# Performance work log

Hardware: AMD Instinct MI355X
Metric: run time of the kernel (lower is better)

Reference implementation:

```python
import jax, jax.numpy as jnp
import numpy as np

B, S, PLM, G = 8, 2048, 768, 256
N_WM, E_WM = 50000, 800000
N_F, E_F = B * S, 131072
K = 4


def _gnn(h, src, dst, Ws, bs, n_nodes):
    # simple GCN-style message passing: aggregate neighbor features via
    # gather (h[src]) + scatter-add (segment_sum), then linear + relu.
    for W, b in zip(Ws, bs):
        m = jax.ops.segment_sum(h[src], dst, num_segments=n_nodes)  # [n, g]
        h = jax.nn.relu((h + m) @ W + b)
    return h


def setup_inputs() -> dict:
    key = jax.random.key(0)
    ks = jax.random.split(key, 16)
    std = 0.02
    inp = {
        "text_embeddings": jax.random.normal(ks[0], (B, S, PLM), jnp.float32),
        "wm_x": jax.random.normal(ks[1], (N_WM, G), jnp.float32),
        "wm_edge_index": jax.random.randint(ks[2], (2, E_WM), 0, N_WM),
        "token2nodepos": jax.random.randint(ks[3], (B * S, K), 0, N_WM),
        "fstm_node_ids": jax.random.randint(ks[4], (N_F,), 0, N_F),
        "fstm_edge_index": jax.random.randint(ks[5], (2, E_F), 0, N_F),
        # extra_emb: nn.Embedding(2, G, padding_idx=0) -> row 0 is zeros
        "extra_emb": jax.random.normal(ks[6], (2, G), jnp.float32).at[0].set(0.0) * std,
        "wm_W1": jax.random.normal(ks[7], (G, G), jnp.float32) * std,
        "wm_b1": jnp.zeros((G,), jnp.float32),
        "wm_W2": jax.random.normal(ks[8], (G, G), jnp.float32) * std,
        "wm_b2": jnp.zeros((G,), jnp.float32),
        "fstm_W1": jax.random.normal(ks[9], (G, G), jnp.float32) * std,
        "fstm_b1": jnp.zeros((G,), jnp.float32),
        "fstm_W2": jax.random.normal(ks[10], (G, G), jnp.float32) * std,
        "fstm_b2": jnp.zeros((G,), jnp.float32),
        "fc1_W": jax.random.normal(ks[11], (G + PLM, G), jnp.float32) * std,
        "fc1_b": jnp.zeros((G,), jnp.float32),
        "fc3_W": jax.random.normal(ks[12], (PLM + 2 * G, PLM), jnp.float32) * std,
        "fc3_b": jnp.zeros((PLM,), jnp.float32),
    }
    return inp


def reference(text_embeddings, wm_x, wm_edge_index, token2nodepos, fstm_node_ids,
              fstm_edge_index, extra_emb, wm_W1, wm_b1, wm_W2, wm_b2,
              fstm_W1, fstm_b1, fstm_W2, fstm_b2, fc1_W, fc1_b, fc3_W, fc3_b):
    # ====== WM ======
    graph_embeddings = _gnn(wm_x, wm_edge_index[0], wm_edge_index[1],
                            (wm_W1, wm_W2), (wm_b1, wm_b2), N_WM)  # [N_WM, G]
    table = jnp.concatenate([extra_emb, graph_embeddings], axis=0)  # [N_WM+2, G]
    # per-token gather-sum over K concept slots (original python loop, vectorized)
    tmp = jnp.sum(table[token2nodepos + 2], axis=1)  # [B*S, G]
    text_flat = text_embeddings.reshape(B * S, PLM)
    graph_text_embed = jnp.concatenate([tmp, text_flat], axis=-1) @ fc1_W + fc1_b  # [B*S, G]
    # ====== FSTM ======
    x = graph_text_embed[fstm_node_ids]  # [B*S, G]
    temporal = _gnn(x, fstm_edge_index[0], fstm_edge_index[1],
                    (fstm_W1, fstm_W2), (fstm_b1, fstm_b2), N_F)
    temporal = temporal.reshape(B, S, G)
    # ====== Final ======
    final_vec = jnp.concatenate(
        [text_embeddings, tmp.reshape(B, S, G), temporal], axis=-1)
    logits = final_vec @ fc3_W + fc3_b  # [B, S, PLM]
    return logits
```

## Files before the change

kernel.cpp:

```cpp
#include <hip/hip_runtime.h>

#define Bsz 8
#define Ssz 2048
#define PLM 768
#define Gd  256
#define N_WM 50000
#define E_WM 800000
#define N_F  16384
#define E_F  131072
#define Kc   4

typedef unsigned short ushort_t;
typedef unsigned int uint_t;
typedef short short8 __attribute__((ext_vector_type(8)));
typedef float f32x4 __attribute__((ext_vector_type(4)));

__device__ __forceinline__ ushort_t f2bf(float f) {
    union { float f; unsigned int u; } v; v.f = f;
    unsigned int r = (v.u + 0x7fffu + ((v.u >> 16) & 1u)) >> 16;
    return (ushort_t)r;
}
__device__ __forceinline__ float bf2f(ushort_t b) {
    union { unsigned int u; float f; } v; v.u = ((unsigned int)b) << 16;
    return v.f;
}
__device__ __forceinline__ float4 bf4f(ushort4 u) {
    return make_float4(bf2f(u.x), bf2f(u.y), bf2f(u.z), bf2f(u.w));
}

__device__ __forceinline__ void gl2lds16(const ushort_t* g, ushort_t* l) {
    __builtin_amdgcn_global_load_lds(
        (const __attribute__((address_space(1))) unsigned int*)g,
        (__attribute__((address_space(3))) unsigned int*)l, 16, 0, 0);
}

#define NSL 8
#define SLW 32

__device__ __forceinline__ void cvt4(const float* __restrict__ in,
                                     ushort_t* __restrict__ out, int i, int n4) {
    if (i < n4) {
        float4 v = ((const float4*)in)[i];
        ushort4 u;
        u.x = f2bf(v.x); u.y = f2bf(v.y); u.z = f2bf(v.z); u.w = f2bf(v.w);
        ((ushort4*)out)[i] = u;
    }
}

__device__ __forceinline__ void cvt4_sm(const float* __restrict__ in,
                                        ushort_t* __restrict__ out, int i, int n4,
                                        int nrows) {
    if (i < n4) {
        float4 v = ((const float4*)in)[i];
        int flat = i * 4;
        int node = flat >> 8, c = flat & 255;
        int s = c >> 5, cc = c & 31;
        ushort4 u;
        u.x = f2bf(v.x); u.y = f2bf(v.y); u.z = f2bf(v.z); u.w = f2bf(v.w);
        *(ushort4*)&out[((size_t)s * nrows + node) * SLW + cc] = u;
    }
}

__device__ __forceinline__ void wtx_tile(const float* __restrict__ W,
                                         ushort_t* __restrict__ Wt,
                                         int K, int N, int tile,
                                         ushort_t (*sm)[65]) {
    int kt = K >> 6;
    int k0 = (tile % kt) << 6;
    int n0 = (tile / kt) << 6;
    int t = threadIdx.x;
    int tr = t >> 6, tc = t & 63;
#pragma unroll
    for (int p = 0; p < 16; ++p) {
        int k = p * 4 + tr;
        sm[k][tc] = f2bf(W[(size_t)(k0 + k) * N + n0 + tc]);
    }
    __syncthreads();
#pragma unroll
    for (int p = 0; p < 16; ++p) {
        int n = p * 4 + tr;
        Wt[(size_t)(n0 + n) * K + k0 + tc] = sm[tc][n];
    }
}

__global__ void conv_all(const float* __restrict__ wm_x, const float* __restrict__ text,
                         const float* __restrict__ extra,
                         const float* __restrict__ W1, const float* __restrict__ W2,
                         const float* __restrict__ W3, const float* __restrict__ W4,
                         const float* __restrict__ W5, const float* __restrict__ W6,
                         ushort_t* __restrict__ Xb, ushort_t* __restrict__ Tx,
                         ushort_t* __restrict__ Exb,
                         ushort_t* __restrict__ T1, ushort_t* __restrict__ T2,
                         ushort_t* __restrict__ T3, ushort_t* __restrict__ T4,
                         ushort_t* __restrict__ T5, ushort_t* __restrict__ T6) {
    __shared__ ushort_t sm[64][65];
    int b = blockIdx.x, t = threadIdx.x;
    if (b < 12500) { cvt4_sm(wm_x, Xb, b * 256 + t, 3200000, N_WM); return; }
    b -= 12500;
    if (b < 12288) { cvt4(text, Tx, b * 256 + t, 3145728); return; }
    b -= 12288;
    if (b < 1) { cvt4(extra, Exb, t, 128); return; }
    b -= 1;
    if (b < 16) { wtx_tile(W1, T1, 256, 256, b, sm); return; }
    b -= 16;
    if (b < 16) { wtx_tile(W2, T2, 256, 256, b, sm); return; }
    b -= 16;
    if (b < 16) { wtx_tile(W3, T3, 256, 256, b, sm); return; }
    b -= 16;
    if (b < 16) { wtx_tile(W4, T4, 256, 256, b, sm); return; }
    b -= 16;
    if (b < 64) { wtx_tile(W5, T5, 1024, 256, b, sm); return; }
    b -= 64;
    wtx_tile(W6, T6, 1280, 768, b, sm);
}

#define WM_P 512
#define WM_CH 1563
#define WM_SHIFT 8
#define FS_P 128
#define FS_CH 1024
#define FS_SHIFT 6

__global__ __launch_bounds__(256) void csr_p1(const int* __restrict__ wm_dst,
                                              const int* __restrict__ f_dst,
                                              int* __restrict__ Cwm,
                                              int* __restrict__ Cfs) {
    __shared__ int hist[256];
    int b = blockIdx.x, t = threadIdx.x;
    hist[t] = 0; __syncthreads();
    if (b < WM_P) {
        int e0 = b * WM_CH, e1 = e0 + WM_CH; if (e1 > E_WM) e1 = E_WM;
        for (int e = e0 + t; e < e1; e += 256)
            atomicAdd(&hist[wm_dst[e] >> WM_SHIFT], 1);
        __syncthreads();
        Cwm[b * 256 + t] = hist[t];
    } else {
        int p = b - WM_P;
        int e0 = p * FS_CH, e1 = e0 + FS_CH;
        for (int e = e0 + t; e < e1; e += 256)
            atomicAdd(&hist[f_dst[e] >> FS_SHIFT], 1);
        __syncthreads();
        Cfs[p * 256 + t] = hist[t];
    }
}

__global__ __launch_bounds__(256) void csr_p2a(int* __restrict__ Cwm, int* __restrict__ BTwm,
                                               int* __restrict__ Cfs, int* __restrict__ BTfs) {
    __shared__ int sm[256];
    int b = blockIdx.x, t = threadIdx.x;
    int* C; int* BT; int P; int bk;
    if (b < 256) { C = Cwm; BT = BTwm; P = WM_P; bk = b; }
    else         { C = Cfs; BT = BTfs; P = FS_P; bk = b - 256; }
    int half = P >> 1;
    int v0 = 0, v1 = 0;
    if (t < half) { v0 = C[(2 * t) * 256 + bk]; v1 = C[(2 * t + 1) * 256 + bk]; }
    int s = v0 + v1;
    sm[t] = s; __syncthreads();
#pragma unroll
    for (int st = 1; st < 256; st <<= 1) {
        int x = (t >= st) ? sm[t - st] : 0;
        __syncthreads();
        sm[t] += x;
        __syncthreads();
    }
    int ex = sm[t] - s;
    if (t < half) {
        C[(2 * t) * 256 + bk] = ex;
        C[(2 * t + 1) * 256 + bk] = ex + v0;
    }
    if (t == 255) BT[bk] = sm[255];
}

__global__ __launch_bounds__(256) void csr_p2b(const int* __restrict__ BTwm,
                                               int* __restrict__ BSwm,
                                               const int* __restrict__ BTfs,
                                               int* __restrict__ BSfs) {
    __shared__ int sm[256];
    int t = threadIdx.x;
    const int* BT = blockIdx.x ? BTfs : BTwm;
    int* BS = blockIdx.x ? BSfs : BSwm;
    int E = blockIdx.x ? E_F : E_WM;
    int v = BT[t];
    sm[t] = v; __syncthreads();
#pragma unroll
    for (int st = 1; st < 256; st <<= 1) {
        int x = (t >= st) ? sm[t - st] : 0;
        __syncthreads();
        sm[t] += x;
        __syncthreads();
    }
    BS[t] = sm[t] - v;
    if (t == 255) BS[256] = E;
}

__global__ __launch_bounds__(256) void csr_p3(const int* __restrict__ wm_src,
                                              const int* __restrict__ wm_dst,
                                              const int* __restrict__ Cwm,
                                              const int* __restrict__ BSwm,
                                              int2* __restrict__ SEwm,
                                              const int* __restrict__ f_src,
                                              const int* __restrict__ f_dst,
                                              const int* __restrict__ Cfs,
                                              const int* __restrict__ BSfs,
                                              int2* __restrict__ SEfs) {
    __shared__ int cur[256];
    int b = blockIdx.x, t = threadIdx.x;
    if (b < WM_P) {
        cur[t] = Cwm[b * 256 + t] + BSwm[t];
        __syncthreads();
        int e0 = b * WM_CH, e1 = e0 + WM_CH; if (e1 > E_WM) e1 = E_WM;
        for (int e = e0 + t; e < e1; e += 256) {
            int d = wm_dst[e], s = wm_src[e];
            int pos = atomicAdd(&cur[d >> WM_SHIFT], 1);
            SEwm[pos] = make_int2(s, d);
        }
    } else {
        int p = b - WM_P;
        cur[t] = Cfs[p * 256 + t] + BSfs[t];
        __syncthreads();
        int e0 = p * FS_CH, e1 = e0 + FS_CH;
        for (int e = e0 + t; e < e1; e += 256) {
            int d = f_dst[e], s = f_src[e];
            int pos = atomicAdd(&cur[d >> FS_SHIFT], 1);
            SEfs[pos] = make_int2(s, d);
        }
    }
}

__global__ __launch_bounds__(256) void csr_p4(const int2* __restrict__ SEwm,
                                              const int* __restrict__ BSwm,
                                              int* __restrict__ wm_off,
                                              int* __restrict__ wm_bkt,
                                              const int2* __restrict__ SEfs,
                                              const int* __restrict__ BSfs,
                                              int* __restrict__ fs_off,
                                              int* __restrict__ fs_bkt) {
    __shared__ int cnt[256];
    __shared__ int sm[256];
    int ob = blockIdx.x, t = threadIdx.x;
    const int2* SE; const int* BS; int* off; int* bkt;
    int b, nb0, n, E, bw;
    if (ob < 256) { SE = SEwm; BS = BSwm; off = wm_off; bkt = wm_bkt;
                    b = ob; nb0 = b << WM_SHIFT; n = N_WM; E = E_WM; bw = 256; }
    else          { SE = SEfs; BS = BSfs; off = fs_off; bkt = fs_bkt;
                    b = ob - 256; nb0 = b << FS_SHIFT; n = N_F; E = E_F; bw = 64; }
    int e0 = BS[b], e1 = BS[b + 1];
    cnt[t] = 0; __syncthreads();
    for (int e = e0 + t; e < e1; e += 256)
        atomicAdd(&cnt[SE[e].y - nb0], 1);
    __syncthreads();
    int v = cnt[t];
    sm[t] = v; __syncthreads();
#pragma unroll
    for (int st = 1; st < 256; st <<= 1) {
        int x = (t >= st) ? sm[t - st] : 0;
        __syncthreads();
        sm[t] += x;
        __syncthreads();
    }
    int ex = sm[t] - v;
    if (t < bw && nb0 + t < n) off[nb0 + t] = e0 + ex;
    if (b == 0 && t == 0) off[n] = E;
    __syncthreads();
    cnt[t] = e0 + ex;
    __syncthreads();
    for (int e = e0 + t; e < e1; e += 256) {
        int2 sd = SE[e];
        int pos = atomicAdd(&cnt[sd.y - nb0], 1);
        bkt[pos] = sd.x;
    }
}

__global__ __launch_bounds__(256) void aggregate_sliced(
        const ushort_t* __restrict__ h, const int* __restrict__ off,
        const int* __restrict__ bucket, ushort_t* __restrict__ hm, int n) {
    int bid = blockIdx.x;
    int s = bid & 7, nb = bid >> 3;
    int wave = threadIdx.x >> 6;
    int lane = threadIdx.x & 63;
    int i = nb * 4 + wave;
    if (i >= n) return;
    int g = lane >> 3;
    int li = lane & 7;
    const ushort4* hp = (const ushort4*)(h + (size_t)s * n * SLW);
    ushort4* op = (ushort4*)(hm + (size_t)s * n * SLW);
    int s0 = off[i], s1 = off[i + 1];
    float ax = 0.f, ay = 0.f, az = 0.f, aw = 0.f;
    int j = s0;
    for (; j + 16 <= s1; j += 16) {
        int b0 = bucket[j + g];
        int b1 = bucket[j + 8 + g];
        ushort4 r0 = hp[(size_t)b0 * 8 + li];
        ushort4 r1 = hp[(size_t)b1 * 8 + li];
        float4 v0 = bf4f(r0), v1 = bf4f(r1);
        ax += v0.x + v1.x; ay += v0.y + v1.y;
        az += v0.z + v1.z; aw += v0.w + v1.w;
    }
    for (; j + 8 <= s1; j += 8) {
        int b0 = bucket[j + g];
        ushort4 r0 = hp[(size_t)b0 * 8 + li];
        float4 v0 = bf4f(r0);
        ax += v0.x; ay += v0.y; az += v0.z; aw += v0.w;
    }
    if (j + g < s1) {
        int b0 = bucket[j + g];
        ushort4 r0 = hp[(size_t)b0 * 8 + li];
        float4 v0 = bf4f(r0);
        ax += v0.x; ay += v0.y; az += v0.z; aw += v0.w;
    }
#pragma unroll
    for (int m = 8; m < 64; m <<= 1) {
        ax += __shfl_xor(ax, m, 64);
        ay += __shfl_xor(ay, m, 64);
        az += __shfl_xor(az, m, 64);
        aw += __shfl_xor(aw, m, 64);
    }
    if (g == 0) {
        float4 dv = bf4f(hp[(size_t)i * 8 + li]);
        ushort4 u;
        u.x = f2bf(ax + dv.x); u.y = f2bf(ay + dv.y);
        u.z = f2bf(az + dv.z); u.w = f2bf(aw + dv.w);
        op[(size_t)i * 8 + li] = u;
    }
}

__global__ void aggregate_kernel(const ushort_t* __restrict__ h,
                                 const int* __restrict__ off,
                                 const int* __restrict__ bucket,
                                 ushort_t* __restrict__ hm, int n) {
    int i = blockIdx.x * 4 + (threadIdx.x >> 6);
    if (i >= n) return;
    int lane = threadIdx.x & 63;
    int s0 = off[i], s1 = off[i + 1];
    const ushort4* hp = (const ushort4*)h;
    float4 acc = bf4f(hp[(size_t)i * 64 + lane]);
    int j = s0;
    for (; j + 8 <= s1; j += 8) {
        int bb[8];
#pragma unroll
        for (int q = 0; q < 8; ++q) bb[q] = bucket[j + q];
        ushort4 rr[8];
#pragma unroll
        for (int q = 0; q < 8; ++q) rr[q] = hp[(size_t)bb[q] * 64 + lane];
#pragma unroll
        for (int q = 0; q < 8; ++q) {
            float4 v = bf4f(rr[q]);
            acc.x += v.x; acc.y += v.y; acc.z += v.z; acc.w += v.w;
        }
    }
    for (; j < s1; ++j) {
        float4 v = bf4f(hp[(size_t)bucket[j] * 64 + lane]);
        acc.x += v.x; acc.y += v.y; acc.z += v.z; acc.w += v.w;
    }
    ushort4 u;
    u.x = f2bf(acc.x); u.y = f2bf(acc.y); u.z = f2bf(acc.z); u.w = f2bf(acc.w);
    ((ushort4*)hm)[(size_t)i * 64 + lane] = u;
}

__global__ void tmp_kernel(const ushort_t* __restrict__ gemb,
                           const ushort_t* __restrict__ extra,
                           const int* __restrict__ t2np,
                           ushort_t* __restrict__ D) {
    int i = blockIdx.x * 4 + (threadIdx.x >> 6);
    int lane = threadIdx.x & 63;
    float4 s = make_float4(0.f, 0.f, 0.f, 0.f);
#pragma unroll
    for (int k = 0; k < Kc; ++k) {
        int idx = t2np[i * Kc + k] + 2;
        const ushort4* row = (idx < 2) ? (const ushort4*)(extra + (size_t)idx * Gd)
                                       : (const ushort4*)(gemb + (size_t)(idx - 2) * Gd);
        float4 v = bf4f(row[lane]);
        s.x += v.x; s.y += v.y; s.z += v.z; s.w += v.w;
    }
    ushort4 u;
    u.x = f2bf(s.x); u.y = f2bf(s.y); u.z = f2bf(s.z); u.w = f2bf(s.w);
    ((ushort4*)D)[(size_t)i * 64 + lane] = u;
}

__global__ void gather_kernel(const ushort_t* __restrict__ Ein,
                              const int* __restrict__ ids,
                              ushort_t* __restrict__ F) {
    int i = blockIdx.x * 4 + (threadIdx.x >> 6);
    int lane = threadIdx.x & 63;
    ((ushort4*)F)[(size_t)i * 64 + lane] =
        ((const ushort4*)Ein)[(size_t)ids[i] * 64 + lane];
}

#define TBK 64
#define GBM 64
#define GBN 128

__device__ __forceinline__ void xcd_swizzle(int& bx, int& by) {
    int gx = gridDim.x;
    int nwg = gx * gridDim.y;
    int orig = by * gx + bx;
    int q = nwg >> 3, r = nwg & 7;
    int xcd = orig & 7, loc = orig >> 3;
    int wg = (xcd < r ? xcd * (q + 1) : r * (q + 1) + (xcd - r) * q) + loc;
    bx = wg % gx;
    by = wg / gx;
}

template <int MODE, int OUTBF, int OUTSM, int BM, int BN>
__global__ __launch_bounds__(256) void mfma_gemm(
    const ushort_t* __restrict__ p0, const ushort_t* __restrict__ p1,
    const ushort_t* __restrict__ p2, const ushort_t* __restrict__ Wt,
    const float* __restrict__ bias, void* __restrict__ Cv,
    int M, int N, int K, int relu) {
    constexpr int MR = BM / 32;
    constexpr int NR = BN / 32;
    constexpr int A_IT = (BM * TBK) / 2048;
    constexpr int B_IT = (BN * TBK) / 2048;
    __shared__ ushort_t As[BM * TBK];
    __shared__ ushort_t Bs[BN * TBK];

    int tid  = threadIdx.x;
    int lane = tid & 63;
    int wave = tid >> 6;
    int wm = (wave >> 1) * (BM / 2), wn = (wave & 1) * (BN / 2);
    int bx = blockIdx.x, by = blockIdx.y;
    xcd_swizzle(bx, by);
    int row0 = by * BM, col0 = bx * BN;
    int l15 = lane & 15, l4 = lane >> 4;

    f32x4 acc[MR][NR];
#pragma unroll
    for (int i = 0; i < MR; ++i)
#pragma unroll
        for (int j = 0; j < NR; ++j)
            acc[i][j] = (f32x4){0.f, 0.f, 0.f, 0.f};

    for (int k0 = 0; k0 < K; k0 += TBK) {
#pragma unroll
        for (int it = 0; it < A_IT; ++it) {
            int eb = it * 2048 + wave * 512;
            int le = eb + lane * 8;
            int r  = le >> 6;
            int kl = (le ^ ((r & 7) << 3)) & 63;
            int grow = row0 + r; if (grow > M - 1) grow = M - 1;
            int gk = k0 + kl;
            const ushort_t* gp;
            if (MODE == 0)
                gp = p0 + (size_t)grow * K + gk;
            else if (MODE == 1)
                gp = p0 + ((size_t)(gk >> 5) * M + grow) * SLW + (gk & 31);
            else if (MODE == 2)
                gp = (gk < 256) ? p0 + (size_t)grow * 256 + gk
                                : p1 + (size_t)grow * 768 + (gk - 256);
            else
                gp = (gk < 768) ? p0 + (size_t)grow * 768 + gk
                   : (gk < 1024) ? p1 + (size_t)grow * 256 + (gk - 768)
                                 : p2 + (size_t)grow * 256 + (gk - 1024);
            gl2lds16(gp, &As[eb]);
        }
#pragma unroll
        for (int it = 0; it < B_IT; ++it) {
            int eb = it * 2048 + wave * 512;
            int le = eb + lane * 8;
            int nl = le >> 6;
            int kl = (le ^ ((nl & 7) << 3)) & 63;
            const ushort_t* gp = Wt + (size_t)(col0 + nl) * K + k0 + kl;
            gl2lds16(gp, &Bs[eb]);
        }
        __syncthreads();

#pragma unroll
        for (int ks = 0; ks < TBK; ks += 32) {
            short8 af[MR], bfr[NR];
#pragma unroll
            for (int mi = 0; mi < MR; ++mi) {
                int row = wm + mi * 16 + l15;
                int col = (ks + l4 * 8) ^ ((row & 7) << 3);
                af[mi] = *(const short8*)&As[row * TBK + col];
            }
#pragma unroll
            for (int ni = 0; ni < NR; ++ni) {
                int row = wn + ni * 16 + l15;
                int col = (ks + l4 * 8) ^ ((row & 7) << 3);
                bfr[ni] = *(const short8*)&Bs[row * TBK + col];
            }
#pragma unroll
            for (int mi = 0; mi < MR; ++mi)
#pragma unroll
                for (int ni = 0; ni < NR; ++ni)
                    acc[mi][ni] = __builtin_amdgcn_mfma_f32_16x16x32_bf16(
                        af[mi], bfr[ni], acc[mi][ni], 0, 0, 0);
        }
        __syncthreads();
    }

#pragma unroll
    for (int ni = 0; ni < NR; ++ni) {
        int c = col0 + wn + ni * 16 + l15;
        float bv = bias[c];
#pragma unroll
        for (int mi = 0; mi < MR; ++mi) {
#pragma unroll
            for (int r = 0; r < 4; ++r) {
                int rr = row0 + wm + mi * 16 + l4 * 4 + r;
                if (rr < M) {
                    float v = acc[mi][ni][r] + bv;
                    if (relu) v = fmaxf(v, 0.f);
                    if (OUTBF) {
                        if (OUTSM)
                            ((ushort_t*)Cv)[((size_t)(c >> 5) * M + rr) * SLW + (c & 31)] = f2bf(v);
                        else
                            ((ushort_t*)Cv)[(size_t)rr * N + c] = f2bf(v);
                    } else {
                        ((float*)Cv)[(size_t)rr * N + c] = v;
                    }
                }
            }
        }
    }
}

extern "C" void kernel_launch(void* const* d_in, const int* in_sizes, int n_in,
                              void* d_out, int out_size, void* d_ws, size_t ws_size,
                              hipStream_t stream) {
    const float* text    = (const float*)d_in[0];
    const float* wm_x    = (const float*)d_in[1];
    const int*   wm_ei   = (const int*)d_in[2];
    const int*   t2np    = (const int*)d_in[3];
    const int*   f_ids   = (const int*)d_in[4];
    const int*   f_ei    = (const int*)d_in[5];
    const float* extra   = (const float*)d_in[6];
    const float* wm_W1   = (const float*)d_in[7];
    const float* wm_b1   = (const float*)d_in[8];
    const float* wm_W2   = (const float*)d_in[9];
    const float* wm_b2   = (const float*)d_in[10];
    const float* fs_W1   = (const float*)d_in[11];
    const float* fs_b1   = (const float*)d_in[12];
    const float* fs_W2   = (const float*)d_in[13];
    const float* fs_b2   = (const float*)d_in[14];
    const float* fc1_W   = (const float*)d_in[15];
    const float* fc1_b   = (const float*)d_in[16];
    const float* fc3_W   = (const float*)d_in[17];
    const float* fc3_b   = (const float*)d_in[18];
    float* out = (float*)d_out;

    ushort_t* Xb  = (ushort_t*)d_ws;
    ushort_t* Ag  = Xb + 12800000;
    ushort_t* Gm  = Ag + 12800000;
    ushort_t* Tx  = Gm + 12800000;
    ushort_t* Dt  = Tx + 12582912;
    ushort_t* Ee  = Dt + 4194304;
    ushort_t* Wv  = Ee + 4194304;
    ushort_t* wt_wm1 = Wv;
    ushort_t* wt_wm2 = wt_wm1 + 65536;
    ushort_t* wt_fs1 = wt_wm2 + 65536;
    ushort_t* wt_fs2 = wt_fs1 + 65536;
    ushort_t* wt_fc1 = wt_fs2 + 65536;
    ushort_t* wt_fc3 = wt_fc1 + 262144;
    ushort_t* Exb    = wt_fc3 + 983040;
    int* wm_off = (int*)(Exb + 512);
    int* fs_off = wm_off + N_WM + 1;
    int* wm_bkt = fs_off + N_F + 1;
    int* fs_bkt = wm_bkt + E_WM;
    int2* SEwm = (int2*)Ag;
    int2* SEfs = SEwm + E_WM;
    int*  Cwm  = (int*)(SEfs + E_F);
    int*  Cfs  = Cwm + WM_P * 256;
    int*  BTwm = Cfs + FS_P * 256;
    int*  BTfs = BTwm + 256;
    int*  BSwm = BTfs + 256;
    int*  BSfs = BSwm + 257;

    ushort_t* h1 = Xb;
    ushort_t* F  = Gm;
    ushort_t* H  = Gm + 4194304;
    ushort_t* T  = Ee;

    const int* wm_src = wm_ei;
    const int* wm_dst = wm_ei + E_WM;
    const int* f_src  = f_ei;
    const int* f_dst  = f_ei + E_F;

    dim3 blk(256);
    dim3 gW(Gd / GBN, (N_WM + GBM - 1) / GBM);
    dim3 gF(Gd / GBN, N_F / GBM);
    dim3 gO(PLM / GBN, N_F / GBM);
    const int gAggW = NSL * ((N_WM + 3) / 4);

    csr_p1<<<WM_P + FS_P, blk, 0, stream>>>(wm_dst, f_dst, Cwm, Cfs);
    csr_p2a<<<512, blk, 0, stream>>>(Cwm, BTwm, Cfs, BTfs);
    csr_p2b<<<2, blk, 0, stream>>>(BTwm, BSwm, BTfs, BSfs);
    csr_p3<<<WM_P + FS_P, blk, 0, stream>>>(wm_src, wm_dst, Cwm, BSwm, SEwm,
                                            f_src, f_dst, Cfs, BSfs, SEfs);
    csr_p4<<<512, blk, 0, stream>>>(SEwm, BSwm, wm_off, wm_bkt,
                                    SEfs, BSfs, fs_off, fs_bkt);

    conv_all<<<25157, blk, 0, stream>>>(wm_x, text, extra,
                                        wm_W1, wm_W2, fs_W1, fs_W2, fc1_W, fc3_W,
                                        Xb, Tx, Exb,
                                        wt_wm1, wt_wm2, wt_fs1, wt_fs2,
                                        wt_fc1, wt_fc3);

    aggregate_sliced<<<gAggW, blk, 0, stream>>>(Xb, wm_off, wm_bkt, Ag, N_WM);
    mfma_gemm<1, 1, 1, GBM, GBN><<<gW, blk, 0, stream>>>(Ag, nullptr, nullptr, wt_wm1,
                                                         wm_b1, h1, N_WM, Gd, Gd, 1);
    aggregate_sliced<<<gAggW, blk, 0, stream>>>(h1, wm_off, wm_bkt, Ag, N_WM);
    mfma_gemm<1, 1, 0, GBM, GBN><<<gW, blk, 0, stream>>>(Ag, nullptr, nullptr, wt_wm2,
                                                         wm_b2, Gm, N_WM, Gd, Gd, 1);
    tmp_kernel<<<N_F / 4, blk, 0, stream>>>(Gm, Exb, t2np, Dt);
    mfma_gemm<2, 1, 0, GBM, GBN><<<gF, blk, 0, stream>>>(Dt, Tx, nullptr, wt_fc1,
                                                         fc1_b, Ee, N_F, Gd, Gd + PLM, 0);
    gather_kernel<<<N_F / 4, blk, 0, stream>>>(Ee, f_ids, F);
    aggregate_kernel<<<N_F / 4, blk, 0, stream>>>(F, fs_off, fs_bkt, Ag, N_F);
    mfma_gemm<0, 1, 0, GBM, GBN><<<gF, blk, 0, stream>>>(Ag, nullptr, nullptr, wt_fs1,
                                                         fs_b1, H, N_F, Gd, Gd, 1);
    aggregate_kernel<<<N_F / 4, blk, 0, stream>>>(H, fs_off, fs_bkt, Ag, N_F);
    mfma_gemm<0, 1, 0, GBM, GBN><<<gF, blk, 0, stream>>>(Ag, nullptr, nullptr, wt_fs2,
                                                         fs_b2, T, N_F, Gd, Gd, 1);
    mfma_gemm<3, 0, 0, GBM, GBN><<<gO, blk, 0, stream>>>(Tx, Dt, T, wt_fc3, fc3_b,
                                                         out, N_F, PLM, PLM + 2 * Gd, 0);
}
```

Before: 642.1 us.

## Map one node per 8-lane group in sliced WM aggregation

Restructures the sliced neighbor aggregation so each 8-lane group handles its own destination node, rather than one wave per node with edges spread across lane groups and a shuffle reduction. Each block now covers 32 nodes, which cuts the grid by a factor of eight, removes the cross-group shuffle reduction and lets every lane write its result. Edge reads are unrolled by four per group. The cost is load imbalance from varying degrees within a wave, and out-of-range nodes are clamped to the last node, which is then written redundantly.

```diff
diff --git a/kernel.cpp b/kernel.cpp
--- a/kernel.cpp
+++ b/kernel.cpp
@@ -275,53 +275,41 @@
         const ushort_t* __restrict__ h, const int* __restrict__ off,
         const int* __restrict__ bucket, ushort_t* __restrict__ hm, int n) {
     int bid = blockIdx.x;
-    int s = bid & 7, nb = bid >> 3;
+    int s = bid & 7, grp = bid >> 3;
     int wave = threadIdx.x >> 6;
     int lane = threadIdx.x & 63;
-    int i = nb * 4 + wave;
-    if (i >= n) return;
-    int g = lane >> 3;
+    int nl = lane >> 3;
     int li = lane & 7;
+    int i = grp * 32 + wave * 8 + nl;
+    if (i >= n) i = n - 1;
     const ushort4* hp = (const ushort4*)(h + (size_t)s * n * SLW);
     ushort4* op = (ushort4*)(hm + (size_t)s * n * SLW);
-    int s0 = off[i], s1 = off[i + 1];
-    float ax = 0.f, ay = 0.f, az = 0.f, aw = 0.f;
-    int j = s0;
-    for (; j + 16 <= s1; j += 16) {
-        int b0 = bucket[j + g];
-        int b1 = bucket[j + 8 + g];
+    int s0 = off[i], deg = off[i + 1] - s0;
+    float4 acc = bf4f(hp[(size_t)i * 8 + li]);
+    int j = 0;
+    for (; j + 4 <= deg; j += 4) {
+        int b0 = bucket[s0 + j + 0];
+        int b1 = bucket[s0 + j + 1];
+        int b2 = bucket[s0 + j + 2];
+        int b3 = bucket[s0 + j + 3];
         ushort4 r0 = hp[(size_t)b0 * 8 + li];
         ushort4 r1 = hp[(size_t)b1 * 8 + li];
-        float4 v0 = bf4f(r0), v1 = bf4f(r1);
-        ax += v0.x + v1.x; ay += v0.y + v1.y;
-        az += v0.z + v1.z; aw += v0.w + v1.w;
-    }
-    for (; j + 8 <= s1; j += 8) {
-        int b0 = bucket[j + g];
-        ushort4 r0 = hp[(size_t)b0 * 8 + li];
-        float4 v0 = bf4f(r0);
-        ax += v0.x; ay += v0.y; az += v0.z; aw += v0.w;
-    }
-    if (j + g < s1) {
-        int b0 = bucket[j + g];
-        ushort4 r0 = hp[(size_t)b0 * 8 + li];
-        float4 v0 = bf4f(r0);
-        ax += v0.x; ay += v0.y; az += v0.z; aw += v0.w;
-    }
-#pragma unroll
-    for (int m = 8; m < 64; m <<= 1) {
-        ax += __shfl_xor(ax, m, 64);
-        ay += __shfl_xor(ay, m, 64);
-        az += __shfl_xor(az, m, 64);
-        aw += __shfl_xor(aw, m, 64);
-    }
-    if (g == 0) {
-        float4 dv = bf4f(hp[(size_t)i * 8 + li]);
-        ushort4 u;
-        u.x = f2bf(ax + dv.x); u.y = f2bf(ay + dv.y);
-        u.z = f2bf(az + dv.z); u.w = f2bf(aw + dv.w);
-        op[(size_t)i * 8 + li] = u;
-    }
+        ushort4 r2 = hp[(size_t)b2 * 8 + li];
+        ushort4 r3 = hp[(size_t)b3 * 8 + li];
+        float4 v0 = bf4f(r0), v1 = bf4f(r1), v2 = bf4f(r2), v3 = bf4f(r3);
+        acc.x += v0.x + v1.x + v2.x + v3.x;
+        acc.y += v0.y + v1.y + v2.y + v3.y;
+        acc.z += v0.z + v1.z + v2.z + v3.z;
+        acc.w += v0.w + v1.w + v2.w + v3.w;
+    }
+    for (; j < deg; ++j) {
+        int b0 = bucket[s0 + j];
+        float4 v0 = bf4f(hp[(size_t)b0 * 8 + li]);
+        acc.x += v0.x; acc.y += v0.y; acc.z += v0.z; acc.w += v0.w;
+    }
+    ushort4 u;
+    u.x = f2bf(acc.x); u.y = f2bf(acc.y); u.z = f2bf(acc.z); u.w = f2bf(acc.w);
+    op[(size_t)i * 8 + li] = u;
 }
 
 __global__ void aggregate_kernel(const ushort_t* __restrict__ h,
@@ -580,7 +568,7 @@
     dim3 gW(Gd / GBN, (N_WM + GBM - 1) / GBM);
     dim3 gF(Gd / GBN, N_F / GBM);
     dim3 gO(PLM / GBN, N_F / GBM);
-    const int gAggW = NSL * ((N_WM + 3) / 4);
+    const int gAggW = NSL * ((N_WM + 31) / 32);
 
     csr_p1<<<WM_P + FS_P, blk, 0, stream>>>(wm_dst, f_dst, Cwm, Cfs);
     csr_p2a<<<512, blk, 0, stream>>>(Cwm, BTwm, Cfs, BTfs);
```

New measurement: 523.5 us. 1.23x faster.
